# Kernel tuning notes

Measured on AMD Instinct MI355X. Metric: run time of the kernel, lower is better.

Reference implementation:

```python
import jax, jax.numpy as jnp
import numpy as np
from jax import lax

SCORE_THRESH = 0.05
NMS_THRESH = 0.5
TOPK = 100
NEG = -1.0  # scores are softmax probs in (0,1); -1 acts as -inf for sorting/top-k


def _iou_matrix(b):
    # b: (R,4) xyxy -> (R,R) pairwise IoU (torchvision convention, no +1)
    area = (b[:, 2] - b[:, 0]) * (b[:, 3] - b[:, 1])
    lt = jnp.maximum(b[:, None, :2], b[None, :, :2])
    rb = jnp.minimum(b[:, None, 2:], b[None, :, 2:])
    wh = jnp.clip(rb - lt, 0.0)
    inter = wh[..., 0] * wh[..., 1]
    union = area[:, None] + area[None, :] - inter
    return inter / jnp.maximum(union, 1e-9)


def _nms_one_class(b_c, s_c):
    # b_c: (R,4), s_c: (R,). Greedy NMS in descending-score order.
    order = jnp.argsort(-s_c)
    b = b_c[order]
    s = s_c[order]
    valid = s > SCORE_THRESH
    iou = _iou_matrix(b)  # (R,R)
    R = b.shape[0]

    def body(i, state):
        keep, active = state
        ki = active[i] & valid[i]
        keep = keep.at[i].set(ki)
        active = active & ~(ki & (iou[i] > NMS_THRESH))
        return keep, active

    keep, _ = lax.fori_loop(0, R, body,
                            (jnp.zeros(R, bool), jnp.ones(R, bool)))
    return b, jnp.where(keep, s, NEG)


def setup_inputs() -> dict:
    key = jax.random.key(0)
    k1, k2, k3, k4, k5 = jax.random.split(key, 5)
    R, K = 1000, 80
    H, W = 800, 1333
    # Well-formed per-class boxes (x1<x2, y1<y2) roughly inside the image.
    cx = jax.random.uniform(k1, (R, K)) * W
    cy = jax.random.uniform(k2, (R, K)) * H
    w = jax.random.uniform(k3, (R, K)) * 200.0 + 10.0
    h = jax.random.uniform(k4, (R, K)) * 200.0 + 10.0
    boxes = jnp.stack([cx - w / 2, cy - h / 2, cx + w / 2, cy + h / 2],
                      axis=-1).reshape(R, K * 4).astype(jnp.float32)
    scores = jax.nn.softmax(jax.random.normal(k5, (R, K + 1)) * 2.0, axis=-1)
    return {"boxes": boxes, "scores": scores.astype(jnp.float32),
            "im_h": H, "im_w": W}


def reference(boxes, scores, im_h, im_w):
    R = boxes.shape[0]
    s = scores[:, :-1]            # (R,K) drop background column
    K = s.shape[1]
    b = boxes.reshape(R, K, 4)
    # clip to image (x in [0,W], y in [0,H])
    x = jnp.clip(b[..., 0::2], 0.0, float(im_w))
    y = jnp.clip(b[..., 1::2], 0.0, float(im_h))
    b = jnp.stack([x[..., 0], y[..., 0], x[..., 1], y[..., 1]], axis=-1)
    # per-class batched NMS, vmapped over the K class axis
    bb, ss = jax.vmap(_nms_one_class, in_axes=(1, 1))(b, s)  # (K,R,4),(K,R)
    classes = jnp.broadcast_to(jnp.arange(K, dtype=jnp.int32)[:, None], ss.shape)
    # global top-k over all surviving (class, box) candidates
    top_s, top_i = lax.top_k(ss.reshape(-1), TOPK)
    top_b = bb.reshape(-1, 4)[top_i]
    top_c = classes.reshape(-1)[top_i]
    dets = jnp.concatenate([top_b, top_s[:, None]], axis=-1)  # (TOPK,5)
    return dets, top_c
```

## Files before the change

kernel.cpp:

```cpp
#include <hip/hip_runtime.h>
#include <hip/hip_bf16.h>

#define R      1000
#define K      80
#define KP1    81
#define CAND   100
#define NC     (K*CAND)
#define VCAP   256
#define SCORE_THRESH 0.05f
#define NMS_THRESH   0.5f

typedef unsigned long long u64;

__device__ unsigned g_ctr = 0;

__device__ __forceinline__ unsigned int ordf(float f) {
    unsigned int u = __float_as_uint(f);
    return (u & 0x80000000u) ? ~u : (u | 0x80000000u);
}
__device__ __forceinline__ float unordf(unsigned int o) {
    unsigned int u = (o & 0x80000000u) ? (o ^ 0x80000000u) : ~o;
    return __uint_as_float(u);
}

__device__ __forceinline__ void st_agent_u64(u64* p, u64 v) {
    __hip_atomic_store(p, v, __ATOMIC_RELAXED, __HIP_MEMORY_SCOPE_AGENT);
}
__device__ __forceinline__ u64 ld_agent_u64(const u64* p) {
    return __hip_atomic_load(p, __ATOMIC_RELAXED, __HIP_MEMORY_SCOPE_AGENT);
}
__device__ __forceinline__ void st_box(float4* p, float4 b) {
    union { float f[2]; u64 u; } lo, hi;
    lo.f[0] = b.x; lo.f[1] = b.y; hi.f[0] = b.z; hi.f[1] = b.w;
    st_agent_u64((u64*)p, lo.u);
    st_agent_u64((u64*)p + 1, hi.u);
}
__device__ __forceinline__ float4 ld_box(const float4* p) {
    union { float f[2]; u64 u; } lo, hi;
    lo.u = ld_agent_u64((const u64*)p);
    hi.u = ld_agent_u64((const u64*)p + 1);
    return make_float4(lo.f[0], lo.f[1], hi.f[0], hi.f[1]);
}

template<int NR>
__device__ __forceinline__ void pipeline(
    int k, int tid, int lane, int w, int V,
    u64* skey, const float4* sbox, float4* sboxs, u64* mat,
    u64* __restrict__ cand_key, float4* __restrict__ cand_box)
{
    const u64 lt_mask = (1ull << lane) - 1ull;
    constexpr int N = NR * 64;

    float sc[NR];
    if (w == 0) {
        u64 key[NR];
        #pragma unroll
        for (int r = 0; r < NR; ++r) key[r] = skey[r * 64 + lane];

        #pragma unroll
        for (int size = 2; size <= N; size <<= 1) {
            #pragma unroll
            for (int stride = size >> 1; stride > 0; stride >>= 1) {
                if (stride >= 64) {
                    const int rs = stride >> 6;
                    #pragma unroll
                    for (int r = 0; r < NR; ++r) {
                        if ((r & rs) == 0 && (r | rs) < NR) {
                            const int r2 = r | rs;
                            const bool desc = (((r * 64) & size) == 0);
                            u64 a = key[r], b = key[r2];
                            bool sw = desc ? (a < b) : (a > b);
                            if (sw) { key[r] = b; key[r2] = a; }
                        }
                    }
                } else {
                    #pragma unroll
                    for (int r = 0; r < NR; ++r) {
                        u64 part = __shfl_xor(key[r], stride, 64);
                        bool desc = (((r * 64 + lane) & size) == 0);
                        bool lower = ((lane & stride) == 0);
                        bool takeMax = (lower == desc);
                        bool pgt = part > key[r];
                        key[r] = (takeMax == pgt) ? part : key[r];
                    }
                }
            }
        }

        #pragma unroll
        for (int r = 0; r < NR; ++r) {
            int i = r * 64 + lane;
            u64 kk = key[r];
            sc[r] = unordf((unsigned)(kk >> 32));
            float4 bb = make_float4(0.f, 0.f, 0.f, 0.f);
            if (i < V) bb = sbox[0xFFFFFFFFu - (unsigned)kk];
            sboxs[i] = bb;
        }
    }
    __syncthreads();

    float4 bx[NR]; float area[NR];
    #pragma unroll
    for (int r = 0; r < NR; ++r) {
        float4 bb = sboxs[r * 64 + lane];
        bx[r] = bb;
        area[r] = (bb.z - bb.x) * (bb.w - bb.y);
    }

    const int Vq = (V + 3) >> 2;
    int jbeg = w * Vq;
    int jend = jbeg + Vq; if (jend > V) jend = V;
    #pragma unroll 2
    for (int j = jbeg; j < jend; ++j) {
        float4 bj = sboxs[j];
        float areaB = (bj.z - bj.x) * (bj.w - bj.y);
        #pragma unroll
        for (int r = 0; r < NR; ++r) {
            float ltx = fmaxf(bx[r].x, bj.x), lty = fmaxf(bx[r].y, bj.y);
            float rbx = fminf(bx[r].z, bj.z), rby = fminf(bx[r].w, bj.w);
            float ww = fmaxf(rbx - ltx, 0.f), hh = fmaxf(rby - lty, 0.f);
            float inter = ww * hh;
            float uni = area[r] + areaB - inter;
            float iou = inter / fmaxf(uni, 1e-9f);
            mat[j * NR + r] = __ballot(iou > NMS_THRESH);
        }
    }
    __syncthreads();

    if (w != 0) return;

    u64 kept[NR];
    #pragma unroll
    for (int r = 0; r < NR; ++r) kept[r] = 0ull;
    u64 cur[NR];
    #pragma unroll
    for (int r = 0; r < NR; ++r) cur[r] = mat[r];

    int j = 0;
    #pragma unroll
    for (int jc = 0; jc < NR; ++jc) {
        int jmax = V - jc * 64;
        if (jmax > 64) jmax = 64;
        for (int jl = 0; jl < jmax; ++jl, ++j) {
            u64 nxt[NR];
            #pragma unroll
            for (int r = 0; r < NR; ++r) nxt[r] = mat[(j + 1) * NR + r];
            u64 hit = 0ull;
            #pragma unroll
            for (int r = 0; r < NR; ++r) hit |= cur[r] & kept[r];
            if (hit == 0ull) kept[jc] |= (1ull << jl);
            #pragma unroll
            for (int r = 0; r < NR; ++r) cur[r] = nxt[r];
        }
    }

    unsigned pre = 0;
    u64* ck = cand_key + (size_t)k * CAND;
    float4* cb = cand_box + (size_t)k * CAND;
    #pragma unroll
    for (int r = 0; r < NR; ++r) {
        u64 m = kept[r];
        bool mine = (m >> lane) & 1ull;
        unsigned rank = pre + (unsigned)__popcll(m & lt_mask);
        if (mine && rank < CAND) {
            unsigned c = (unsigned)(k * CAND + rank);
            st_agent_u64(&ck[rank], ((u64)ordf(sc[r]) << 32) | (u64)(0xFFFFFFFFu - c));
            st_box(&cb[rank], bx[r]);
        }
        pre += (unsigned)__popcll(m);
    }
    unsigned T100 = pre < CAND ? pre : CAND;
    for (unsigned s2 = T100 + (unsigned)lane; s2 < CAND; s2 += 64)
        st_agent_u64(&ck[s2], 0ull);
}

__global__ __launch_bounds__(256, 1) void fused_kernel(
    const float* __restrict__ boxes, const float* __restrict__ scores,
    const int* __restrict__ imh, const int* __restrict__ imw,
    u64* __restrict__ cand_key, float4* __restrict__ cand_box,
    float* __restrict__ out)
{
    const int k = blockIdx.x, tid = threadIdx.x;
    const int lane = tid & 63, w = tid >> 6;

    __shared__ u64    skey[VCAP];
    __shared__ float4 sbox[VCAP];
    __shared__ float4 sboxs[VCAP];
    __shared__ u64    mat[(VCAP + 1) * 4];
    __shared__ unsigned cnt16[16];
    __shared__ int lastf;
    __shared__ unsigned hist[4][264];
    __shared__ unsigned wsum[4];
    __shared__ u64 Psh;
    __shared__ u64 packsh[4];
    __shared__ unsigned remsh, cntsh;
    __shared__ int donesh;
    __shared__ u64 Wl[128];

    skey[tid] = 0ull;
    const float Wf = (float)(*imw), Hf = (float)(*imh);

    float sv[4]; bool val[4]; unsigned posl[4];
    #pragma unroll
    for (int t = 0; t < 4; ++t) {
        int i = w * 256 + t * 64 + lane;
        float s = -1.f;
        if (i < R) s = scores[i * KP1 + k];
        bool v = s > SCORE_THRESH;
        u64 m = __ballot(v);
        sv[t] = s; val[t] = v;
        posl[t] = (unsigned)__popcll(m & ((1ull << lane) - 1ull));
        if (lane == 0) cnt16[w * 4 + t] = (unsigned)__popcll(m);
    }
    __syncthreads();

    unsigned base4[4] = {0, 0, 0, 0};
    unsigned total = 0;
    #pragma unroll
    for (int x = 0; x < 16; ++x) {
        unsigned cc = cnt16[x];
        #pragma unroll
        for (int t = 0; t < 4; ++t) if (x < w * 4 + t) base4[t] += cc;
        total += cc;
    }
    const int V = total < VCAP ? (int)total : VCAP;

    #pragma unroll
    for (int t = 0; t < 4; ++t) {
        if (val[t]) {
            unsigned pos = base4[t] + posl[t];
            if (pos < VCAP) {
                int i = w * 256 + t * 64 + lane;
                skey[pos] = ((u64)ordf(sv[t]) << 32) | (u64)(0xFFFFFFFFu - pos);
                float4 bb = *(const float4*)(boxes + (size_t)i * (K * 4) + (size_t)k * 4);
                bb.x = fminf(fmaxf(bb.x, 0.f), Wf);
                bb.y = fminf(fmaxf(bb.y, 0.f), Hf);
                bb.z = fminf(fmaxf(bb.z, 0.f), Wf);
                bb.w = fminf(fmaxf(bb.w, 0.f), Hf);
                sbox[pos] = bb;
            }
        }
    }
    __syncthreads();

    if (V > 0) {
        if (V <= 64)       pipeline<1>(k, tid, lane, w, V, skey, sbox, sboxs, mat, cand_key, cand_box);
        else if (V <= 128) pipeline<2>(k, tid, lane, w, V, skey, sbox, sboxs, mat, cand_key, cand_box);
        else               pipeline<4>(k, tid, lane, w, V, skey, sbox, sboxs, mat, cand_key, cand_box);
    } else {
        if (w == 0)
            for (int s2 = lane; s2 < CAND; s2 += 64)
                st_agent_u64(&cand_key[(size_t)k * CAND + s2], 0ull);
        __syncthreads();
        __syncthreads();
    }
    __syncthreads();

    if (tid == 0) {
        unsigned old = __hip_atomic_fetch_add(&g_ctr, 1u, __ATOMIC_RELAXED, __HIP_MEMORY_SCOPE_AGENT);
        lastf = ((old % (unsigned)K) == (unsigned)(K - 1)) ? 1 : 0;
    }
    __syncthreads();
    if (!lastf) return;

    u64 keyv[32];
    #pragma unroll
    for (int j = 0; j < 32; ++j) {
        int idx = tid + 256 * j;
        keyv[j] = (idx < NC) ? ld_agent_u64(&cand_key[idx]) : 0ull;
    }

    {
        u64 pack = 0ull;
        #pragma unroll
        for (int j = 0; j < 32; ++j) {
            u64 kk = keyv[j];
            if (kk != 0ull) {
                unsigned b7 = (unsigned)(kk >> 56);
                pack += (b7 == 0xBFu) ? (1ull << 42) : (b7 == 0xBEu) ? (1ull << 21) : 1ull;
            }
        }
        #pragma unroll
        for (int off = 1; off < 64; off <<= 1) pack += __shfl_xor(pack, off, 64);
        if (lane == 0) packsh[w] = pack;
        __syncthreads();
        if (tid == 0) {
            u64 tot = packsh[0] + packsh[1] + packsh[2] + packsh[3];
            unsigned cBF = (unsigned)(tot >> 42) & 0x1FFFFFu;
            unsigned cBE = (unsigned)(tot >> 21) & 0x1FFFFFu;
            unsigned rem = CAND - 1;
            unsigned b, v;
            if (rem < cBF)            { b = 0xBFu; v = cBF; }
            else if (rem < cBF + cBE) { b = 0xBEu; v = cBE; rem -= cBF; }
            else                      { b = 0xBDu; v = (unsigned)tot & 0x1FFFFFu; rem -= cBF + cBE; }
            Psh = (u64)b << 56;
            remsh = rem;
            cntsh = 0;
            donesh = (v == rem + 1) ? 1 : 0;
        }
        __syncthreads();
    }

    const int plist[5] = {6, 5, 4, 1, 0};
    for (int pi = 0; pi < 5; ++pi) {
        if (donesh) break;
        const int p = plist[pi];
        const int shift = 8 * p;
        #pragma unroll
        for (int ww = 0; ww < 4; ++ww) hist[ww][tid] = 0;
        __syncthreads();

        u64 pfx = Psh;
        unsigned rem = remsh;
        u64 hmask = ~0ull << (shift + 8);
        #pragma unroll
        for (int j = 0; j < 32; ++j) {
            u64 kk = keyv[j];
            if (kk != 0ull && ((kk ^ pfx) & hmask) == 0ull)
                atomicAdd(&hist[w][(unsigned)(kk >> shift) & 0xFFu], 1u);
        }
        __syncthreads();

        int b = 255 - tid;
        unsigned v = hist[0][b] + hist[1][b] + hist[2][b] + hist[3][b];
        unsigned inc = v;
        #pragma unroll
        for (int off = 1; off < 64; off <<= 1) {
            unsigned t2 = __shfl_up(inc, off);
            if (lane >= off) inc += t2;
        }
        if (lane == 63) wsum[w] = inc;
        __syncthreads();
        unsigned woff = 0;
        #pragma unroll
        for (int ww = 0; ww < 4; ++ww) if (ww < w) woff += wsum[ww];
        inc += woff;
        unsigned cumG = inc - v;
        if (v > 0 && rem >= cumG && rem < cumG + v) {
            u64 np = Psh | ((u64)(unsigned)b << shift);
            if (p == 4) np |= 0xFFFF0000ull;
            unsigned rem_new = rem - cumG;
            Psh = np;
            remsh = rem_new;
            donesh = (v == rem_new + 1) ? 1 : 0;
        }
        __syncthreads();
    }

    const u64 T = Psh;
    #pragma unroll
    for (int j = 0; j < 32; ++j) {
        u64 kk = keyv[j];
        if (kk >= T && kk != 0ull) {
            unsigned pos = atomicAdd(&cntsh, 1u);
            if (pos < 128) Wl[pos] = kk;
        }
    }
    __syncthreads();

    if (tid < CAND) {
        u64 my = Wl[tid];
        int r = 0;
        for (int j = 0; j < CAND; ++j) r += (Wl[j] > my) ? 1 : 0;
        unsigned c = 0xFFFFFFFFu - (unsigned)my;
        float s = unordf((unsigned)(my >> 32));
        float4 bb = ld_box(&cand_box[c]);
        out[r * 5 + 0] = bb.x;
        out[r * 5 + 1] = bb.y;
        out[r * 5 + 2] = bb.z;
        out[r * 5 + 3] = bb.w;
        out[r * 5 + 4] = s;
        out[500 + r]   = (float)(c / CAND);
    }
}

extern "C" void kernel_launch(void* const* d_in, const int* in_sizes, int n_in,
                              void* d_out, int out_size, void* d_ws, size_t ws_size,
                              hipStream_t stream) {
    const float* boxes  = (const float*)d_in[0];
    const float* scores = (const float*)d_in[1];
    const int*   imh    = (const int*)d_in[2];
    const int*   imw    = (const int*)d_in[3];
    float* out = (float*)d_out;

    u64*    cand_key = (u64*)d_ws;
    float4* cand_box = (float4*)((char*)d_ws + 65536);

    fused_kernel<<<K, 256, 0, stream>>>(boxes, scores, imh, imw,
                                        cand_key, cand_box, out);
}
```

Measured before the change: 23.50 us.

## Replace single-wave bitonic sort with block-wide rank sort and hoist box loads

The per-class bitonic sort, which ran on one wavefront, is replaced by a parallel rank sort: each of up to V threads counts how many keys beat its own and scatters its box and score to that position. Box loads from global memory are issued right after the score loads, before the first barrier, so their latency overlaps the ballot and prefix work. The pipeline is split into a matrix-build step and a scan/emit step, and scores are kept in a new shared array. The rank sort does O(V) shared reads per thread instead of log² shuffle stages, which may cost more when V is large.

```diff
diff --git a/kernel.cpp b/kernel.cpp
--- a/kernel.cpp
+++ b/kernel.cpp
@@ -43,62 +43,9 @@
 }
 
 template<int NR>
-__device__ __forceinline__ void pipeline(
-    int k, int tid, int lane, int w, int V,
-    u64* skey, const float4* sbox, float4* sboxs, u64* mat,
-    u64* __restrict__ cand_key, float4* __restrict__ cand_box)
+__device__ __forceinline__ void build_matrix(
+    int lane, int w, int V, const float4* sboxs, u64* mat)
 {
-    const u64 lt_mask = (1ull << lane) - 1ull;
-    constexpr int N = NR * 64;
-
-    float sc[NR];
-    if (w == 0) {
-        u64 key[NR];
-        #pragma unroll
-        for (int r = 0; r < NR; ++r) key[r] = skey[r * 64 + lane];
-
-        #pragma unroll
-        for (int size = 2; size <= N; size <<= 1) {
-            #pragma unroll
-            for (int stride = size >> 1; stride > 0; stride >>= 1) {
-                if (stride >= 64) {
-                    const int rs = stride >> 6;
-                    #pragma unroll
-                    for (int r = 0; r < NR; ++r) {
-                        if ((r & rs) == 0 && (r | rs) < NR) {
-                            const int r2 = r | rs;
-                            const bool desc = (((r * 64) & size) == 0);
-                            u64 a = key[r], b = key[r2];
-                            bool sw = desc ? (a < b) : (a > b);
-                            if (sw) { key[r] = b; key[r2] = a; }
-                        }
-                    }
-                } else {
-                    #pragma unroll
-                    for (int r = 0; r < NR; ++r) {
-                        u64 part = __shfl_xor(key[r], stride, 64);
-                        bool desc = (((r * 64 + lane) & size) == 0);
-                        bool lower = ((lane & stride) == 0);
-                        bool takeMax = (lower == desc);
-                        bool pgt = part > key[r];
-                        key[r] = (takeMax == pgt) ? part : key[r];
-                    }
-                }
-            }
-        }
-
-        #pragma unroll
-        for (int r = 0; r < NR; ++r) {
-            int i = r * 64 + lane;
-            u64 kk = key[r];
-            sc[r] = unordf((unsigned)(kk >> 32));
-            float4 bb = make_float4(0.f, 0.f, 0.f, 0.f);
-            if (i < V) bb = sbox[0xFFFFFFFFu - (unsigned)kk];
-            sboxs[i] = bb;
-        }
-    }
-    __syncthreads();
-
     float4 bx[NR]; float area[NR];
     #pragma unroll
     for (int r = 0; r < NR; ++r) {
@@ -106,7 +53,6 @@
         bx[r] = bb;
         area[r] = (bb.z - bb.x) * (bb.w - bb.y);
     }
-
     const int Vq = (V + 3) >> 2;
     int jbeg = w * Vq;
     int jend = jbeg + Vq; if (jend > V) jend = V;
@@ -125,9 +71,15 @@
             mat[j * NR + r] = __ballot(iou > NMS_THRESH);
         }
     }
-    __syncthreads();
-
-    if (w != 0) return;
+}
+
+template<int NR>
+__device__ __forceinline__ void scan_emit(
+    int k, int lane, int V,
+    const float4* sboxs, const float* sscs, const u64* mat,
+    u64* __restrict__ cand_key, float4* __restrict__ cand_box)
+{
+    const u64 lt_mask = (1ull << lane) - 1ull;
 
     u64 kept[NR];
     #pragma unroll
@@ -164,8 +116,9 @@
         unsigned rank = pre + (unsigned)__popcll(m & lt_mask);
         if (mine && rank < CAND) {
             unsigned c = (unsigned)(k * CAND + rank);
-            st_agent_u64(&ck[rank], ((u64)ordf(sc[r]) << 32) | (u64)(0xFFFFFFFFu - c));
-            st_box(&cb[rank], bx[r]);
+            float s = sscs[r * 64 + lane];
+            st_agent_u64(&ck[rank], ((u64)ordf(s) << 32) | (u64)(0xFFFFFFFFu - c));
+            st_box(&cb[rank], sboxs[r * 64 + lane]);
         }
         pre += (unsigned)__popcll(m);
     }
@@ -186,6 +139,7 @@
     __shared__ u64    skey[VCAP];
     __shared__ float4 sbox[VCAP];
     __shared__ float4 sboxs[VCAP];
+    __shared__ float  sscs[VCAP];
     __shared__ u64    mat[(VCAP + 1) * 4];
     __shared__ unsigned cnt16[16];
     __shared__ int lastf;
@@ -197,20 +151,30 @@
     __shared__ int donesh;
     __shared__ u64 Wl[128];
 
-    skey[tid] = 0ull;
     const float Wf = (float)(*imw), Hf = (float)(*imh);
 
-    float sv[4]; bool val[4]; unsigned posl[4];
+    float sv[4];
     #pragma unroll
     for (int t = 0; t < 4; ++t) {
         int i = w * 256 + t * 64 + lane;
-        float s = -1.f;
-        if (i < R) s = scores[i * KP1 + k];
-        bool v = s > SCORE_THRESH;
+        sv[t] = (i < R) ? scores[i * KP1 + k] : -1.f;
+    }
+    bool val[4]; unsigned posl[4];
+    #pragma unroll
+    for (int t = 0; t < 4; ++t) {
+        bool v = sv[t] > SCORE_THRESH;
         u64 m = __ballot(v);
-        sv[t] = s; val[t] = v;
+        val[t] = v;
         posl[t] = (unsigned)__popcll(m & ((1ull << lane) - 1ull));
         if (lane == 0) cnt16[w * 4 + t] = (unsigned)__popcll(m);
+    }
+    float4 rb[4];
+    #pragma unroll
+    for (int t = 0; t < 4; ++t) {
+        if (val[t]) {
+            int i = w * 256 + t * 64 + lane;
+            rb[t] = *(const float4*)(boxes + (size_t)i * (K * 4) + (size_t)k * 4);
+        }
     }
     __syncthreads();
 
@@ -230,9 +194,8 @@
         if (val[t]) {
             unsigned pos = base4[t] + posl[t];
             if (pos < VCAP) {
-                int i = w * 256 + t * 64 + lane;
                 skey[pos] = ((u64)ordf(sv[t]) << 32) | (u64)(0xFFFFFFFFu - pos);
-                float4 bb = *(const float4*)(boxes + (size_t)i * (K * 4) + (size_t)k * 4);
+                float4 bb = rb[t];
                 bb.x = fminf(fmaxf(bb.x, 0.f), Wf);
                 bb.y = fminf(fmaxf(bb.y, 0.f), Hf);
                 bb.z = fminf(fmaxf(bb.z, 0.f), Wf);
@@ -243,16 +206,30 @@
     }
     __syncthreads();
 
+    if (tid < V) {
+        u64 my = skey[tid];
+        int rank = 0;
+        #pragma unroll 4
+        for (int j = 0; j < V; ++j) rank += (skey[j] > my) ? 1 : 0;
+        sboxs[rank] = sbox[tid];
+        sscs[rank]  = unordf((unsigned)(my >> 32));
+    }
+    __syncthreads();
+
     if (V > 0) {
-        if (V <= 64)       pipeline<1>(k, tid, lane, w, V, skey, sbox, sboxs, mat, cand_key, cand_box);
-        else if (V <= 128) pipeline<2>(k, tid, lane, w, V, skey, sbox, sboxs, mat, cand_key, cand_box);
-        else               pipeline<4>(k, tid, lane, w, V, skey, sbox, sboxs, mat, cand_key, cand_box);
-    } else {
-        if (w == 0)
+        if (V <= 64)       build_matrix<1>(lane, w, V, sboxs, mat);
+        else if (V <= 128) build_matrix<2>(lane, w, V, sboxs, mat);
+        else               build_matrix<4>(lane, w, V, sboxs, mat);
+    }
+    __syncthreads();
+
+    if (w == 0) {
+        if (V == 0) {
             for (int s2 = lane; s2 < CAND; s2 += 64)
                 st_agent_u64(&cand_key[(size_t)k * CAND + s2], 0ull);
-        __syncthreads();
-        __syncthreads();
+        } else if (V <= 64)  scan_emit<1>(k, lane, V, sboxs, sscs, mat, cand_key, cand_box);
+        else if (V <= 128)   scan_emit<2>(k, lane, V, sboxs, sscs, mat, cand_key, cand_box);
+        else                 scan_emit<4>(k, lane, V, sboxs, sscs, mat, cand_key, cand_box);
     }
     __syncthreads();
 
```

Result: no change. 23.48 us (-0.1%).
